# Performance work log

Measured on AMD Instinct MI355X. Metric: run time of the kernel, lower is better.

The kernel has to match this reference:

```python
import jax, jax.numpy as jnp
import numpy as np

D_MODEL = 1024


def setup_inputs() -> dict:
    key = jax.random.key(0)
    ks = jax.random.split(key, 7)
    x = jax.random.normal(ks[0], (4, 2048, D_MODEL), dtype=jnp.float32)
    scale = 1.0 / np.sqrt(D_MODEL)
    Wq = jax.random.normal(ks[1], (D_MODEL, D_MODEL), dtype=jnp.float32) * scale
    bq = jnp.zeros((D_MODEL,), dtype=jnp.float32)
    Wk = jax.random.normal(ks[2], (D_MODEL, D_MODEL), dtype=jnp.float32) * scale
    bk = jnp.zeros((D_MODEL,), dtype=jnp.float32)
    Wv = jax.random.normal(ks[3], (D_MODEL, D_MODEL), dtype=jnp.float32) * scale
    bv = jnp.zeros((D_MODEL,), dtype=jnp.float32)
    return {"x": x, "Wq": Wq, "bq": bq, "Wk": Wk, "bk": bk, "Wv": Wv, "bv": bv}


def reference(x, Wq, bq, Wk, bk, Wv, bv):
    # Linear layers: y = x @ W^T + b (torch nn.Linear convention)
    q = jnp.einsum("bsd,ed->bse", x, Wq) + bq
    k = jnp.einsum("bsd,ed->bse", x, Wk) + bk
    v = jnp.einsum("bsd,ed->bse", x, Wv) + bv
    d_k = q.shape[-1]
    inv_sqrt_dk = 1.0 / jnp.sqrt(jnp.float32(d_k))
    # [B, S, S] score matrix, softmax over keys, then AV
    score = jnp.einsum("bqd,bkd->bqk", q, k) * inv_sqrt_dk
    attn = jax.nn.softmax(score, axis=-1)
    out = jnp.einsum("bqk,bkd->bqd", attn, v)
    return out
```

## Files before the change

kernel.cpp:

```cpp
#include <hip/hip_runtime.h>
#include <hip/hip_bf16.h>


typedef __hip_bfloat16 bf16;
typedef __attribute__((ext_vector_type(8))) short bf16x8;
typedef __attribute__((ext_vector_type(16))) float f32x16;
typedef __attribute__((ext_vector_type(4))) short short4v;

__device__ __forceinline__ void gload16(const bf16* g, bf16* l) {
  __builtin_amdgcn_global_load_lds(
      (const __attribute__((address_space(1))) void*)g,
      (__attribute__((address_space(3))) void*)l, 16, 0, 0);
}

__global__ __launch_bounds__(256)
void cast_f32_to_bf16(const float* __restrict__ in, bf16* __restrict__ out) {
  long i = ((long)blockIdx.x * blockDim.x + threadIdx.x) * 4;
  float4 f = *(const float4*)(in + i);
  bf16 tmp[4];
  tmp[0] = __float2bfloat16(f.x);
  tmp[1] = __float2bfloat16(f.y);
  tmp[2] = __float2bfloat16(f.z);
  tmp[3] = __float2bfloat16(f.w);
  *(short4v*)(out + i) = *(short4v*)tmp;
}

template<int OMODE>
__global__ __launch_bounds__(256, 3)
void gemm_bt(const bf16* __restrict__ A, const bf16* __restrict__ Bt,
             const float* __restrict__ b0, const float* __restrict__ b1,
             const float* __restrict__ b2, void* __restrict__ Cout,
             int K, int lda, int ldb, int ldc, float scale,
             long sA, long sB, long sC)
{
  __shared__ __align__(16) bf16 As[128 * 64];
  __shared__ __align__(16) bf16 Bs[128 * 64];
  const int tid = threadIdx.x;
  const int z = blockIdx.z;
  const bf16* Ab = A + (long)z * sA;
  const bf16* Bb = Bt + (long)z * sB;
  const long bm = (long)blockIdx.x * 128;
  const long bn = (long)blockIdx.y * 128;
  const int wid = tid >> 6;
  const int lane = tid & 63;
  const int wr = (wid >> 1) * 64;
  const int wc = (wid & 1) * 64;
  const int fr = lane & 31;
  const int kh = lane >> 5;

  f32x16 acc[2][2];
#pragma unroll
  for (int m = 0; m < 2; ++m)
#pragma unroll
    for (int n = 0; n < 2; ++n)
      acc[m][n] = (f32x16){0.f,0.f,0.f,0.f,0.f,0.f,0.f,0.f,
                           0.f,0.f,0.f,0.f,0.f,0.f,0.f,0.f};

  for (int k0 = 0; k0 < K; k0 += 64) {
#pragma unroll
    for (int i = 0; i < 4; ++i) {
      const int c = (i << 8) + tid;
      const int r = c >> 3;
      const int j = (c & 7) ^ (r & 7);
      const int ldsch = (i << 8) + (wid << 6);
      gload16(Ab + (long)(bm + r) * lda + k0 + (j << 3), As + ldsch * 8);
      gload16(Bb + (long)(bn + r) * ldb + k0 + (j << 3), Bs + ldsch * 8);
    }
    __syncthreads();
#pragma unroll
    for (int ks = 0; ks < 4; ++ks) {
      bf16x8 af[2], bfv[2];
#pragma unroll
      for (int m = 0; m < 2; ++m) {
        const int row_l = wr + (m << 5) + fr;
        const int js = ((ks << 1) + kh) ^ (row_l & 7);
        af[m] = *(const bf16x8*)&As[(row_l << 6) + (js << 3)];
      }
#pragma unroll
      for (int n = 0; n < 2; ++n) {
        const int row_l = wc + (n << 5) + fr;
        const int js = ((ks << 1) + kh) ^ (row_l & 7);
        bfv[n] = *(const bf16x8*)&Bs[(row_l << 6) + (js << 3)];
      }
#pragma unroll
      for (int m = 0; m < 2; ++m)
#pragma unroll
        for (int n = 0; n < 2; ++n)
          acc[m][n] = __builtin_amdgcn_mfma_f32_32x32x16_bf16(
              af[m], bfv[n], acc[m][n], 0, 0, 0);
    }
    __syncthreads();
  }

#pragma unroll
  for (int m = 0; m < 2; ++m) {
#pragma unroll
    for (int n = 0; n < 2; ++n) {
      const long col = bn + wc + (n << 5) + fr;
#pragma unroll
      for (int g = 0; g < 4; ++g) {
        const long row0 = bm + wr + (m << 5) + (g << 3) + (kh << 2);
        if constexpr (OMODE == 0) {
          float* C = (float*)Cout + (long)z * sC;
#pragma unroll
          for (int rr = 0; rr < 4; ++rr)
            C[(row0 + rr) * ldc + col] = acc[m][n][(g << 2) + rr] * scale;
        } else if constexpr (OMODE == 1) {
          bf16* C = (bf16*)Cout + (long)z * sC;
#pragma unroll
          for (int rr = 0; rr < 4; ++rr)
            C[(row0 + rr) * ldc + col] =
                __float2bfloat16(acc[m][n][(g << 2) + rr] * scale);
        } else {
          const float* bias = (z == 0) ? b0 : (z == 1) ? b1 : b2;
          const float bias_v = bias[col];
          if (z < 2) {
            bf16* C = (bf16*)Cout + (long)z * 8192 * 1024;
#pragma unroll
            for (int rr = 0; rr < 4; ++rr)
              C[(row0 + rr) * 1024 + col] =
                  __float2bfloat16(acc[m][n][(g << 2) + rr] + bias_v);
          } else {
            bf16* C = (bf16*)Cout + 2L * 8192 * 1024;
            const long bb = row0 >> 11;
            const long s0 = row0 & 2047;
            bf16 tmp[4];
#pragma unroll
            for (int rr = 0; rr < 4; ++rr)
              tmp[rr] = __float2bfloat16(acc[m][n][(g << 2) + rr] + bias_v);
            *(short4v*)&C[(bb * 1024 + col) * 2048 + s0] = *(short4v*)tmp;
          }
        }
      }
    }
  }
}

__global__ __launch_bounds__(256)
void softmax_bf16(bf16* __restrict__ S) {
  bf16* row = S + (size_t)blockIdx.x * 2048;
  const int tid = threadIdx.x;
  __shared__ float redA[4], redB[4];
  bf16x8 in = *(const bf16x8*)(row + (tid << 3));
  float v[8];
  float mx = -1e30f;
#pragma unroll
  for (int i = 0; i < 8; ++i) {
    v[i] = __bfloat162float(((const bf16*)&in)[i]);
    mx = fmaxf(mx, v[i]);
  }
#pragma unroll
  for (int o = 32; o; o >>= 1) mx = fmaxf(mx, __shfl_xor(mx, o));
  if ((tid & 63) == 0) redA[tid >> 6] = mx;
  __syncthreads();
  mx = fmaxf(fmaxf(redA[0], redA[1]), fmaxf(redA[2], redA[3]));
  float sum = 0.f;
#pragma unroll
  for (int i = 0; i < 8; ++i) {
    v[i] = __expf(v[i] - mx);
    sum += v[i];
  }
#pragma unroll
  for (int o = 32; o; o >>= 1) sum += __shfl_xor(sum, o);
  if ((tid & 63) == 0) redB[tid >> 6] = sum;
  __syncthreads();
  sum = redB[0] + redB[1] + redB[2] + redB[3];
  const float inv = 1.f / sum;
  bf16 tmp[8];
#pragma unroll
  for (int i = 0; i < 8; ++i) tmp[i] = __float2bfloat16(v[i] * inv);
  *(bf16x8*)(row + (tid << 3)) = *(bf16x8*)tmp;
}

extern "C" void kernel_launch(void* const* d_in, const int* in_sizes, int n_in,
                              void* d_out, int out_size, void* d_ws, size_t ws_size,
                              hipStream_t stream) {
  const float* x  = (const float*)d_in[0];
  const float* Wq = (const float*)d_in[1];
  const float* bq = (const float*)d_in[2];
  const float* Wk = (const float*)d_in[3];
  const float* bk = (const float*)d_in[4];
  const float* Wv = (const float*)d_in[5];
  const float* bv = (const float*)d_in[6];
  float* out = (float*)d_out;

  const int B = 4, S = 2048, D = 1024;
  const int M = B * S;

  bf16* xb  = (bf16*)d_ws;
  bf16* wqb = xb + (size_t)M * D;
  bf16* qb  = wqb + 3 * (size_t)D * D;
  bf16* kb  = qb + (size_t)M * D;
  bf16* vtb = kb + (size_t)M * D;
  bf16* sc  = vtb + (size_t)M * D;

  size_t avail = ws_size - ((size_t)((char*)sc - (char*)d_ws));
  int nb = (int)(avail / ((size_t)S * S * 2));
  if (nb > B) nb = B;
  if (nb < 1) nb = 1;

  cast_f32_to_bf16<<<dim3(M * D / 1024), 256, 0, stream>>>(x, xb);
  cast_f32_to_bf16<<<dim3(D * D / 1024), 256, 0, stream>>>(Wq, wqb);
  cast_f32_to_bf16<<<dim3(D * D / 1024), 256, 0, stream>>>(Wk, wqb + (size_t)D * D);
  cast_f32_to_bf16<<<dim3(D * D / 1024), 256, 0, stream>>>(Wv, wqb + 2 * (size_t)D * D);

  gemm_bt<3><<<dim3(M / 128, D / 128, 3), 256, 0, stream>>>(
      xb, wqb, bq, bk, bv, qb, D, D, D, D, 1.f, 0, (long)D * D, 0);

  const float iscale = 1.0f / 32.0f;
  for (int g = 0; g < B; g += nb) {
    const int gn = (g + nb <= B) ? nb : (B - g);
    gemm_bt<1><<<dim3(S / 128, S / 128, gn), 256, 0, stream>>>(
        qb + (size_t)g * S * D, kb + (size_t)g * S * D, nullptr, nullptr, nullptr,
        sc, D, D, D, S, iscale, (long)S * D, (long)S * D, (long)S * S);
    softmax_bf16<<<dim3(gn * S), 256, 0, stream>>>(sc);
    gemm_bt<0><<<dim3(S / 128, D / 128, gn), 256, 0, stream>>>(
        sc, vtb + (size_t)g * D * S, nullptr, nullptr, nullptr,
        out + (size_t)g * S * D, S, S, S, D, 1.f,
        (long)S * S, (long)D * S, (long)S * D);
  }
}
```

Before: 190.8 us.

## Switch GEMM to 16x16x32 MFMA tiles and merge weight casts

Measured after the change: 169.7 us. 11.0% less time.

```diff
diff --git a/kernel.cpp b/kernel.cpp
--- a/kernel.cpp
+++ b/kernel.cpp
@@ -4,7 +4,7 @@
 
 typedef __hip_bfloat16 bf16;
 typedef __attribute__((ext_vector_type(8))) short bf16x8;
-typedef __attribute__((ext_vector_type(16))) float f32x16;
+typedef __attribute__((ext_vector_type(4))) float f32x4;
 typedef __attribute__((ext_vector_type(4))) short short4v;
 
 __device__ __forceinline__ void gload16(const bf16* g, bf16* l) {
@@ -23,6 +23,20 @@
   tmp[2] = __float2bfloat16(f.z);
   tmp[3] = __float2bfloat16(f.w);
   *(short4v*)(out + i) = *(short4v*)tmp;
+}
+
+__global__ __launch_bounds__(256)
+void cast3_f32_to_bf16(const float* __restrict__ w0, const float* __restrict__ w1,
+                       const float* __restrict__ w2, bf16* __restrict__ out) {
+  const float* src = (blockIdx.y == 0) ? w0 : (blockIdx.y == 1) ? w1 : w2;
+  long i = ((long)blockIdx.x * blockDim.x + threadIdx.x) * 4;
+  float4 f = *(const float4*)(src + i);
+  bf16 tmp[4];
+  tmp[0] = __float2bfloat16(f.x);
+  tmp[1] = __float2bfloat16(f.y);
+  tmp[2] = __float2bfloat16(f.z);
+  tmp[3] = __float2bfloat16(f.w);
+  *(short4v*)(out + (long)blockIdx.y * 1024 * 1024 + i) = *(short4v*)tmp;
 }
 
 template<int OMODE>
@@ -45,16 +59,15 @@
   const int lane = tid & 63;
   const int wr = (wid >> 1) * 64;
   const int wc = (wid & 1) * 64;
-  const int fr = lane & 31;
-  const int kh = lane >> 5;
-
-  f32x16 acc[2][2];
-#pragma unroll
-  for (int m = 0; m < 2; ++m)
-#pragma unroll
-    for (int n = 0; n < 2; ++n)
-      acc[m][n] = (f32x16){0.f,0.f,0.f,0.f,0.f,0.f,0.f,0.f,
-                           0.f,0.f,0.f,0.f,0.f,0.f,0.f,0.f};
+  const int l15 = lane & 15;
+  const int kg = lane >> 4;
+
+  f32x4 acc[4][4];
+#pragma unroll
+  for (int m = 0; m < 4; ++m)
+#pragma unroll
+    for (int n = 0; n < 4; ++n)
+      acc[m][n] = (f32x4){0.f, 0.f, 0.f, 0.f};
 
   for (int k0 = 0; k0 < K; k0 += 64) {
 #pragma unroll
@@ -68,68 +81,64 @@
     }
     __syncthreads();
 #pragma unroll
-    for (int ks = 0; ks < 4; ++ks) {
-      bf16x8 af[2], bfv[2];
-#pragma unroll
-      for (int m = 0; m < 2; ++m) {
-        const int row_l = wr + (m << 5) + fr;
-        const int js = ((ks << 1) + kh) ^ (row_l & 7);
+    for (int kk = 0; kk < 2; ++kk) {
+      bf16x8 af[4], bfv[4];
+#pragma unroll
+      for (int m = 0; m < 4; ++m) {
+        const int row_l = wr + (m << 4) + l15;
+        const int js = ((kk << 2) + kg) ^ (row_l & 7);
         af[m] = *(const bf16x8*)&As[(row_l << 6) + (js << 3)];
       }
 #pragma unroll
-      for (int n = 0; n < 2; ++n) {
-        const int row_l = wc + (n << 5) + fr;
-        const int js = ((ks << 1) + kh) ^ (row_l & 7);
+      for (int n = 0; n < 4; ++n) {
+        const int row_l = wc + (n << 4) + l15;
+        const int js = ((kk << 2) + kg) ^ (row_l & 7);
         bfv[n] = *(const bf16x8*)&Bs[(row_l << 6) + (js << 3)];
       }
 #pragma unroll
-      for (int m = 0; m < 2; ++m)
-#pragma unroll
-        for (int n = 0; n < 2; ++n)
-          acc[m][n] = __builtin_amdgcn_mfma_f32_32x32x16_bf16(
+      for (int m = 0; m < 4; ++m)
+#pragma unroll
+        for (int n = 0; n < 4; ++n)
+          acc[m][n] = __builtin_amdgcn_mfma_f32_16x16x32_bf16(
               af[m], bfv[n], acc[m][n], 0, 0, 0);
     }
     __syncthreads();
   }
 
 #pragma unroll
-  for (int m = 0; m < 2; ++m) {
-#pragma unroll
-    for (int n = 0; n < 2; ++n) {
-      const long col = bn + wc + (n << 5) + fr;
-#pragma unroll
-      for (int g = 0; g < 4; ++g) {
-        const long row0 = bm + wr + (m << 5) + (g << 3) + (kh << 2);
-        if constexpr (OMODE == 0) {
-          float* C = (float*)Cout + (long)z * sC;
+  for (int m = 0; m < 4; ++m) {
+    const long row0 = bm + wr + (m << 4) + (kg << 2);
+#pragma unroll
+    for (int n = 0; n < 4; ++n) {
+      const long col = bn + wc + (n << 4) + l15;
+      if constexpr (OMODE == 0) {
+        float* C = (float*)Cout + (long)z * sC;
+#pragma unroll
+        for (int rr = 0; rr < 4; ++rr)
+          C[(row0 + rr) * ldc + col] = acc[m][n][rr] * scale;
+      } else if constexpr (OMODE == 1) {
+        bf16* C = (bf16*)Cout + (long)z * sC;
+#pragma unroll
+        for (int rr = 0; rr < 4; ++rr)
+          C[(row0 + rr) * ldc + col] = __float2bfloat16(acc[m][n][rr] * scale);
+      } else {
+        const float* bias = (z == 0) ? b0 : (z == 1) ? b1 : b2;
+        const float bias_v = bias[col];
+        if (z < 2) {
+          bf16* C = (bf16*)Cout + (long)z * 8192 * 1024;
 #pragma unroll
           for (int rr = 0; rr < 4; ++rr)
-            C[(row0 + rr) * ldc + col] = acc[m][n][(g << 2) + rr] * scale;
-        } else if constexpr (OMODE == 1) {
-          bf16* C = (bf16*)Cout + (long)z * sC;
+            C[(row0 + rr) * 1024 + col] =
+                __float2bfloat16(acc[m][n][rr] + bias_v);
+        } else {
+          bf16* C = (bf16*)Cout + 2L * 8192 * 1024;
+          const long bb = row0 >> 11;
+          const long s0 = row0 & 2047;
+          bf16 tmp[4];
 #pragma unroll
           for (int rr = 0; rr < 4; ++rr)
-            C[(row0 + rr) * ldc + col] =
-                __float2bfloat16(acc[m][n][(g << 2) + rr] * scale);
-        } else {
-          const float* bias = (z == 0) ? b0 : (z == 1) ? b1 : b2;
-          const float bias_v = bias[col];
-          if (z < 2) {
-            bf16* C = (bf16*)Cout + (long)z * 8192 * 1024;
-#pragma unroll
-            for (int rr = 0; rr < 4; ++rr)
-              C[(row0 + rr) * 1024 + col] =
-                  __float2bfloat16(acc[m][n][(g << 2) + rr] + bias_v);
-          } else {
-            bf16* C = (bf16*)Cout + 2L * 8192 * 1024;
-            const long bb = row0 >> 11;
-            const long s0 = row0 & 2047;
-            bf16 tmp[4];
-#pragma unroll
-            for (int rr = 0; rr < 4; ++rr)
-              tmp[rr] = __float2bfloat16(acc[m][n][(g << 2) + rr] + bias_v);
-            *(short4v*)&C[(bb * 1024 + col) * 2048 + s0] = *(short4v*)tmp;
-          }
+            tmp[rr] = __float2bfloat16(acc[m][n][rr] + bias_v);
+          *(short4v*)&C[(bb * 1024 + col) * 2048 + s0] = *(short4v*)tmp;
         }
       }
     }
@@ -200,9 +209,7 @@
   if (nb < 1) nb = 1;
 
   cast_f32_to_bf16<<<dim3(M * D / 1024), 256, 0, stream>>>(x, xb);
-  cast_f32_to_bf16<<<dim3(D * D / 1024), 256, 0, stream>>>(Wq, wqb);
-  cast_f32_to_bf16<<<dim3(D * D / 1024), 256, 0, stream>>>(Wk, wqb + (size_t)D * D);
-  cast_f32_to_bf16<<<dim3(D * D / 1024), 256, 0, stream>>>(Wv, wqb + 2 * (size_t)D * D);
+  cast3_f32_to_bf16<<<dim3(D * D / 1024, 3), 256, 0, stream>>>(Wq, Wk, Wv, wqb);
 
   gemm_bt<3><<<dim3(M / 128, D / 128, 3), 256, 0, stream>>>(
       xb, wqb, bq, bk, bv, qb, D, D, D, D, 1.f, 0, (long)D * D, 0);
```
